# Optimization experiments

Measured on AMD Instinct MI355X. Metric: run time of the kernel, lower is better.

Reference implementation:

```python
import jax, jax.numpy as jnp
import numpy as np

B, S, D, H, NB = 512, 200, 256, 4, 2
DH = D // H
N_ITEMS = 100001  # item_num + 1 (padding idx 0)
EPS = 1e-8


def _ln(x, g, b):
    m = x.mean(-1, keepdims=True)
    v = ((x - m) ** 2).mean(-1, keepdims=True)
    return (x - m) / jnp.sqrt(v + EPS) * g + b


def setup_inputs() -> dict:
    key = jax.random.key(0)
    ks = jax.random.split(key, 20)
    f32 = jnp.float32
    item_emb = jax.random.normal(ks[0], (N_ITEMS, D), f32) * 0.02
    item_emb = item_emb.at[0].set(0.0)  # padding_idx=0
    pos_emb = jax.random.normal(ks[1], (S, D), f32) * 0.02
    inp = {
        'item_emb': item_emb,
        'pos_emb': pos_emb,
        'ln1_g': jnp.ones((NB, D), f32),
        'ln1_b': jnp.zeros((NB, D), f32),
        'in_w': jax.random.normal(ks[2], (NB, 3 * D, D), f32) * 0.02,
        'in_b': jnp.zeros((NB, 3 * D), f32),
        'out_w': jax.random.normal(ks[3], (NB, D, D), f32) * 0.02,
        'out_b': jnp.zeros((NB, D), f32),
        'ln2_g': jnp.ones((NB, D), f32),
        'ln2_b': jnp.zeros((NB, D), f32),
        'c1_w': jax.random.normal(ks[4], (NB, D, D), f32) * 0.02,
        'c1_b': jnp.zeros((NB, D), f32),
        'c2_w': jax.random.normal(ks[5], (NB, D, D), f32) * 0.02,
        'c2_b': jnp.zeros((NB, D), f32),
        'last_g': jnp.ones((D,), f32),
        'last_b': jnp.zeros((D,), f32),
        'user_ids': jax.random.randint(ks[6], (B,), 0, 10000),
        'log_seqs': jax.random.randint(ks[7], (B, S), 0, N_ITEMS),
        'pos_seqs': jax.random.randint(ks[8], (B, S), 0, N_ITEMS),
        'neg_seqs': jax.random.randint(ks[9], (B, S), 0, N_ITEMS),
    }
    return inp


def reference(item_emb, pos_emb, ln1_g, ln1_b, in_w, in_b, out_w, out_b,
              ln2_g, ln2_b, c1_w, c1_b, c2_w, c2_b, last_g, last_b,
              user_ids, log_seqs, pos_seqs, neg_seqs):
    seqs = item_emb[log_seqs] * jnp.asarray(D ** 0.5, item_emb.dtype)
    seqs = seqs + pos_emb[None, :, :]  # positions = arange(S)
    tl_mask = (log_seqs != 0)[..., None].astype(seqs.dtype)  # [B,S,1]
    seqs = seqs * tl_mask
    causal = jnp.tril(jnp.ones((S, S), bool))  # True = attend
    scale = 1.0 / np.sqrt(DH)
    for i in range(NB):
        Q = _ln(seqs, ln1_g[i], ln1_b[i])
        q = (Q @ in_w[i, :D].T + in_b[i, :D]).reshape(B, S, H, DH)
        k = (seqs @ in_w[i, D:2 * D].T + in_b[i, D:2 * D]).reshape(B, S, H, DH)
        v = (seqs @ in_w[i, 2 * D:].T + in_b[i, 2 * D:]).reshape(B, S, H, DH)
        scores = jnp.einsum('bqhd,bkhd->bhqk', q, k) * scale
        scores = jnp.where(causal[None, None], scores, -jnp.inf)
        attn = jax.nn.softmax(scores, axis=-1)
        o = jnp.einsum('bhqk,bkhd->bqhd', attn, v).reshape(B, S, D)
        o = o @ out_w[i].T + out_b[i]
        seqs = Q + o  # residual is on layernormed Q (as in source)
        seqs = _ln(seqs, ln2_g[i], ln2_b[i])
        h1 = jax.nn.relu(seqs @ c1_w[i].T + c1_b[i])
        seqs = (h1 @ c2_w[i].T + c2_b[i] + seqs) * tl_mask
    log_feats = _ln(seqs, last_g, last_b)
    pos_embs = item_emb[pos_seqs]
    neg_embs = item_emb[neg_seqs]
    pos_logits = (log_feats * pos_embs).sum(-1)
    neg_logits = (log_feats * neg_embs).sum(-1)
    return (pos_logits, neg_logits)
```

## Files before the change

kernel.cpp:

```cpp
#include <hip/hip_runtime.h>
#include <math.h>

namespace {

constexpr int kB = 512, kS = 200, kD = 256, kH = 4;
constexpr int kM = kB * kS;
constexpr float kEps = 1e-8f;

typedef short bf16x8 __attribute__((ext_vector_type(8)));
typedef float f32x4 __attribute__((ext_vector_type(4)));

__device__ __forceinline__ float bf2f(unsigned short s) {
  return __uint_as_float(((unsigned)s) << 16);
}
__device__ __forceinline__ unsigned cvtpk(float lo, float hi) {
  unsigned r;
  asm("v_cvt_pk_bf16_f32 %0, %1, %2" : "=v"(r) : "v"(lo), "v"(hi));
  return r;
}
__device__ __forceinline__ void gload16(const void* g, void* l) {
  __builtin_amdgcn_global_load_lds(
      (const __attribute__((address_space(1))) void*)g,
      (__attribute__((address_space(3))) void*)l, 16, 0, 0);
}
__device__ __forceinline__ void vm3() { asm volatile("s_waitcnt vmcnt(3)" ::: "memory"); }
__device__ __forceinline__ void vm2() { asm volatile("s_waitcnt vmcnt(2)" ::: "memory"); }
__device__ __forceinline__ void vm0() { asm volatile("s_waitcnt vmcnt(0)" ::: "memory"); }
__device__ __forceinline__ void lk0() { asm volatile("s_waitcnt lgkmcnt(0)" ::: "memory"); }
__device__ __forceinline__ void bar() { asm volatile("s_barrier" ::: "memory"); }

__global__ __launch_bounds__(256) void cvt4_kernel(
    const float* __restrict__ w0, const float* __restrict__ w1,
    const float* __restrict__ w2, const float* __restrict__ w3,
    const float* __restrict__ ln1g,
    unsigned short* __restrict__ o0, unsigned short* __restrict__ o1,
    unsigned short* __restrict__ o2, unsigned short* __restrict__ o3) {
  int blk = blockIdx.x;
  const float* src;
  unsigned short* dst;
  int base;
  bool isin = false;
  if (blk < 384)      { src = w0; dst = o0; base = blk; isin = true; }
  else if (blk < 512) { src = w1; dst = o1; base = blk - 384; }
  else if (blk < 640) { src = w2; dst = o2; base = blk - 512; }
  else                { src = w3; dst = o3; base = blk - 640; }
  int i4 = (base * 256 + threadIdx.x) * 4;
  float4 v = *reinterpret_cast<const float4*>(src + i4);
  if (isin) {
    int layer = (i4 >= 196608) ? 1 : 0;
    int rem = i4 - layer * 196608;
    int n = rem >> 8;
    int k = rem & 255;
    if (n < 256) {
      float4 g = *reinterpret_cast<const float4*>(ln1g + layer * 256 + k);
      v.x *= g.x; v.y *= g.y; v.z *= g.z; v.w *= g.w;
    }
  }
  uint2 o = {cvtpk(v.x, v.y), cvtpk(v.z, v.w)};
  *reinterpret_cast<uint2*>(dst + i4) = o;
}

__global__ __launch_bounds__(64) void s1s2_kernel(
    const float* __restrict__ in_w, const float* __restrict__ in_b,
    const float* __restrict__ ln1g, const float* __restrict__ ln1b,
    float* __restrict__ s1o, float* __restrict__ s2o) {
  int blk = blockIdx.x;
  int layer = blk >> 8, n = blk & 255;
  int k = threadIdx.x * 4;
  float4 w = *reinterpret_cast<const float4*>(in_w + (size_t)layer * 196608 + n * 256 + k);
  float4 g = *reinterpret_cast<const float4*>(ln1g + layer * 256 + k);
  float4 b = *reinterpret_cast<const float4*>(ln1b + layer * 256 + k);
  float a = w.x * g.x + w.y * g.y + w.z * g.z + w.w * g.w;
  float c = w.x * b.x + w.y * b.y + w.z * b.z + w.w * b.w;
#pragma unroll
  for (int o = 32; o >= 1; o >>= 1) { a += __shfl_xor(a, o); c += __shfl_xor(c, o); }
  if (threadIdx.x == 0) {
    s1o[blk] = a;
    s2o[blk] = c + in_b[layer * 768 + n];
  }
}

__global__ __launch_bounds__(512) void embed_kernel(
    const float* __restrict__ item_emb, const float* __restrict__ pos_emb,
    const int* __restrict__ log_seqs, unsigned short* __restrict__ x,
    float2* __restrict__ stats) {
  int bs = blockIdx.x * 8 + (threadIdx.x >> 6);
  int s = bs % kS;
  int idx = log_seqs[bs];
  float msk = (idx != 0) ? 1.f : 0.f;
  int t = threadIdx.x & 63;
  float4 a = reinterpret_cast<const float4*>(item_emb + (size_t)idx * kD)[t];
  float4 p = reinterpret_cast<const float4*>(pos_emb + (size_t)s * kD)[t];
  float v[4];
  v[0] = (a.x * 16.f + p.x) * msk;
  v[1] = (a.y * 16.f + p.y) * msk;
  v[2] = (a.z * 16.f + p.z) * msk;
  v[3] = (a.w * 16.f + p.w) * msk;
  uint2 r = {cvtpk(v[0], v[1]), cvtpk(v[2], v[3])};
  reinterpret_cast<uint2*>(x + (size_t)bs * kD)[t] = r;
  float sm = v[0] + v[1] + v[2] + v[3];
#pragma unroll
  for (int o = 32; o >= 1; o >>= 1) sm += __shfl_xor(sm, o);
  float mean = sm * (1.f / kD);
  float d0 = v[0] - mean, d1 = v[1] - mean, d2 = v[2] - mean, d3 = v[3] - mean;
  float vs = d0 * d0 + d1 * d1 + d2 * d2 + d3 * d3;
#pragma unroll
  for (int o = 32; o >= 1; o >>= 1) vs += __shfl_xor(vs, o);
  if (t == 0) stats[bs] = {mean, rsqrtf(vs * (1.f / kD) + kEps)};
}

template <int MODE, int LN, int G3>
__global__ __launch_bounds__(512, 4) void gemm2(
    const unsigned short* __restrict__ A, int lda,
    const unsigned short* __restrict__ W,
    const float* __restrict__ bias,
    const unsigned short* __restrict__ R, int ldr,
    const float* __restrict__ lng, const float* __restrict__ lnb,
    const float* __restrict__ qg, const float* __restrict__ qb,
    const float2* __restrict__ statsIn,
    const float* __restrict__ s1v, const float* __restrict__ s2v,
    unsigned short* __restrict__ C, int ldc) {
  __shared__ __attribute__((aligned(16))) unsigned short SMEM[36864];
  __shared__ float red1[128][4];
  __shared__ float red2[128][4];
  const int tid = threadIdx.x, lane = tid & 63, wid = tid >> 6;
  int m0, n0;
  if (G3) {
    int g = blockIdx.x / 24, sub = blockIdx.x % 24;
    m0 = (g * 8 + (sub & 7)) * 128;
    n0 = (sub >> 3) * 256;
  } else {
    m0 = blockIdx.x * 128;
    n0 = 0;
  }
  const int wm = wid >> 2, wn = wid & 3;
  const int lrow = lane & 15, kgrp = lane >> 4;
  const int srow = tid >> 2;
  const int sslot = (tid & 3) ^ (srow & 3);
  const unsigned short* gA  = A + (size_t)(m0 + srow) * lda + sslot * 8;
  const unsigned short* gW0 = W + (size_t)(n0 + srow) * kD + sslot * 8;
  const unsigned short* gW1 = gW0 + (size_t)128 * kD;
  const int sa = (kgrp ^ (lrow & 3)) * 8;

#define STAGE(kk, bb)                                                   \
  do {                                                                  \
    gload16(gA + (kk) * 32, &SMEM[(bb) * 4096 + wid * 512]);            \
    gload16(gW0 + (kk) * 32, &SMEM[12288 + (bb) * 8192 + wid * 512]);   \
    gload16(gW1 + (kk) * 32, &SMEM[16384 + (bb) * 8192 + wid * 512]);   \
  } while (0)

  f32x4 acc[4][4] = {};
  STAGE(0, 0);
  STAGE(1, 1);
#pragma unroll
  for (int k = 0; k < 8; ++k) {
    if (k < 7) vm3(); else vm0();
    bar();
    const int buf = k % 3;
    bf16x8 af[4], bfr[4];
#pragma unroll
    for (int x = 0; x < 4; ++x) {
      af[x]  = *reinterpret_cast<const bf16x8*>(
          &SMEM[12288 + buf * 8192 + (wn * 64 + x * 16 + lrow) * 32 + sa]);
      bfr[x] = *reinterpret_cast<const bf16x8*>(
          &SMEM[buf * 4096 + (wm * 64 + x * 16 + lrow) * 32 + sa]);
    }
    if (k + 2 < 8) STAGE(k + 2, (k + 2) % 3);
    __builtin_amdgcn_s_setprio(1);
#pragma unroll
    for (int na = 0; na < 4; ++na)
#pragma unroll
      for (int mb = 0; mb < 4; ++mb)
        acc[na][mb] = __builtin_amdgcn_mfma_f32_16x16x32_bf16(
            af[na], bfr[mb], acc[na][mb], 0, 0, 0);
    __builtin_amdgcn_s_setprio(0);
  }
#undef STAGE
  __syncthreads();
  const bool qpath = (MODE == 4) && (n0 == 0);
  float2 st[4];
  if (MODE == 5 || (MODE == 4 && n0 == 0)) {
#pragma unroll
    for (int mb = 0; mb < 4; ++mb)
      st[mb] = statsIn[m0 + wm * 64 + mb * 16 + lrow];
  }

  auto computeX = [&](int na, int mb, float x[4]) {
    const int gcol = n0 + wn * 64 + na * 16 + kgrp * 4;
    const f32x4 v = acc[na][mb];
    if (MODE == 4 && qpath) {
      float4 t1 = *reinterpret_cast<const float4*>(s1v + gcol);
      float4 t2 = *reinterpret_cast<const float4*>(s2v + gcol);
      const float s1f[4] = {t1.x, t1.y, t1.z, t1.w};
      const float s2f[4] = {t2.x, t2.y, t2.z, t2.w};
#pragma unroll
      for (int r = 0; r < 4; ++r)
        x[r] = st[mb].y * (v[r] - st[mb].x * s1f[r]) + s2f[r];
      return;
    }
    float4 b4 = *reinterpret_cast<const float4*>(bias + gcol);
    const float bx[4] = {b4.x, b4.y, b4.z, b4.w};
    if (MODE == 4) {
#pragma unroll
      for (int r = 0; r < 4; ++r) x[r] = v[r] + bx[r];
    } else {
      int m = m0 + wm * 64 + mb * 16 + lrow;
      ushort4 rv = *reinterpret_cast<const ushort4*>(R + (size_t)m * ldr + gcol);
      const unsigned short* rs = reinterpret_cast<const unsigned short*>(&rv);
      float4 t1 = *reinterpret_cast<const float4*>(qg + gcol);
      float4 t2 = *reinterpret_cast<const float4*>(qb + gcol);
      const float g4[4] = {t1.x, t1.y, t1.z, t1.w};
      const float qb4[4] = {t2.x, t2.y, t2.z, t2.w};
#pragma unroll
      for (int r = 0; r < 4; ++r) {
        float q = (bf2f(rs[r]) - st[mb].x) * st[mb].y * g4[r] + qb4[r];
        x[r] = v[r] + bx[r] + q;
      }
    }
  };

  float mean[4], inv[4];
  if (LN) {
    float sA[4] = {0.f, 0.f, 0.f, 0.f}, sB[4] = {0.f, 0.f, 0.f, 0.f};
#pragma unroll
    for (int na = 0; na < 4; ++na)
#pragma unroll
      for (int mb = 0; mb < 4; ++mb) {
        float x[4];
        computeX(na, mb, x);
#pragma unroll
        for (int r = 0; r < 4; ++r) { sA[mb] += x[r]; sB[mb] += x[r] * x[r]; }
      }
#pragma unroll
    for (int mb = 0; mb < 4; ++mb) {
      sA[mb] += __shfl_xor(sA[mb], 16); sA[mb] += __shfl_xor(sA[mb], 32);
      sB[mb] += __shfl_xor(sB[mb], 16); sB[mb] += __shfl_xor(sB[mb], 32);
    }
    if (kgrp == 0) {
#pragma unroll
      for (int mb = 0; mb < 4; ++mb) {
        int rl = wm * 64 + mb * 16 + lrow;
        red1[rl][wn] = sA[mb];
        red2[rl][wn] = sB[mb];
      }
    }
    __syncthreads();
#pragma unroll
    for (int mb = 0; mb < 4; ++mb) {
      int rl = wm * 64 + mb * 16 + lrow;
      float4 p1 = *reinterpret_cast<const float4*>(red1[rl]);
      float4 p2 = *reinterpret_cast<const float4*>(red2[rl]);
      float t1 = p1.x + p1.y + p1.z + p1.w;
      float t2 = p2.x + p2.y + p2.z + p2.w;
      float mu = t1 * (1.f / 256.f);
      float var = t2 * (1.f / 256.f) - mu * mu;
      mean[mb] = mu;
      inv[mb] = rsqrtf(fmaxf(var, 0.f) + kEps);
    }
  }

  unsigned short* eb = &SMEM[wid * 3072];
  const int rr = lane >> 2, c8 = (lane & 3) * 8;
#pragma unroll
  for (int hh = 0; hh < 2; ++hh) {
    lk0();
#pragma unroll
    for (int mbl = 0; mbl < 2; ++mbl) {
      int mb = hh * 2 + mbl;
#pragma unroll
      for (int na = 0; na < 4; ++na) {
        float x[4];
        computeX(na, mb, x);
        if (LN == 1) {
          int gcol = n0 + wn * 64 + na * 16 + kgrp * 4;
          float4 g4v = *reinterpret_cast<const float4*>(lng + gcol);
          float4 b4v = *reinterpret_cast<const float4*>(lnb + gcol);
          x[0] = (x[0] - mean[mb]) * inv[mb] * g4v.x + b4v.x;
          x[1] = (x[1] - mean[mb]) * inv[mb] * g4v.y + b4v.y;
          x[2] = (x[2] - mean[mb]) * inv[mb] * g4v.z + b4v.z;
          x[3] = (x[3] - mean[mb]) * inv[mb] * g4v.w + b4v.w;
        }
        uint2 o = {cvtpk(x[0], x[1]), cvtpk(x[2], x[3])};
        *reinterpret_cast<uint2*>(&eb[(mbl * 16 + lrow) * 72 + na * 16 + kgrp * 4]) = o;
      }
    }
    lk0();
#pragma unroll
    for (int rh = 0; rh < 2; ++rh) {
      int row = rh * 16 + rr;
      uint4 d0 = *reinterpret_cast<const uint4*>(&eb[row * 72 + c8]);
      uint4 d1 = *reinterpret_cast<const uint4*>(&eb[row * 72 + 32 + c8]);
      size_t gbase = (size_t)(m0 + wm * 64 + hh * 32 + row) * ldc + (n0 + wn * 64 + c8);
      *reinterpret_cast<uint4*>(C + gbase) = d0;
      *reinterpret_cast<uint4*>(C + gbase + 32) = d1;
    }
  }
}

template <int LAST>
__global__ __launch_bounds__(512, 4) void ffn_fused(
    const unsigned short* __restrict__ A, int lda,
    const unsigned short* __restrict__ W1, const float* __restrict__ b1,
    const unsigned short* __restrict__ W2, const float* __restrict__ b2,
    const int* __restrict__ logseq,
    const float* __restrict__ lng, const float* __restrict__ lnb,
    float2* __restrict__ statsOut,
    const float* __restrict__ iembf, const int* __restrict__ posq,
    const int* __restrict__ negq, float* __restrict__ outlg,
    unsigned short* __restrict__ C, int ldc) {
  __shared__ __attribute__((aligned(16))) unsigned short SMEM[36864];
  __shared__ float red1[64][4];
  __shared__ float red2[64][4];
  const int tid = threadIdx.x, lane = tid & 63, wid = tid >> 6;
  const int m0 = blockIdx.x * 64;
  const int wm = wid >> 2, wn = wid & 3;
  const int lrow = lane & 15, kgrp = lane >> 4;
  unsigned short* As = SMEM;
  unsigned short* Ws = SMEM + 4096;
  unsigned short* H1 = SMEM + 20480;
  const int arow = (wid & 3) * 16 + (lane >> 2);
  const int aslot = (lane & 3) ^ (arow & 3);
  const unsigned short* gA = A + (size_t)(m0 + arow) * lda + aslot * 8;
  const int wrow0 = wid * 32 + (lane >> 2);
  const int wrow1 = wrow0 + 16;
  const int ws0 = (lane & 3) ^ (wrow0 & 3);
  const int ws1 = (lane & 3) ^ (wrow1 & 3);
  const unsigned short* gW10 = W1 + wrow0 * 256 + ws0 * 8;
  const unsigned short* gW11 = W1 + wrow1 * 256 + ws1 * 8;
  const unsigned short* gW20 = W2 + wrow0 * 256 + ws0 * 8;
  const unsigned short* gW21 = W2 + wrow1 * 256 + ws1 * 8;
  const int sa = (kgrp ^ (lrow & 3)) * 8;
  const f32x4 zero = {0.f, 0.f, 0.f, 0.f};

#define STG1(kk, bb)                                               \
  do {                                                             \
    if (wid < 4) gload16(gA + (kk) * 32, &As[(bb) * 2048 + wid * 512]); \
    gload16(gW10 + (kk) * 32, &Ws[(bb) * 8192 + wid * 1024]);      \
    gload16(gW11 + (kk) * 32, &Ws[(bb) * 8192 + wid * 1024 + 512]);\
  } while (0)

  f32x4 acc[4][2] = {};
  STG1(0, 0);
  STG1(1, 1);
#pragma unroll
  for (int k = 0; k < 8; ++k) {
    if (k < 7) { if (wid < 4) vm3(); else vm2(); } else vm0();
    bar();
    const int buf = k & 1;
    bf16x8 af[4], bfr[2];
#pragma unroll
    for (int x = 0; x < 4; ++x)
      af[x] = *reinterpret_cast<const bf16x8*>(
          &Ws[buf * 8192 + (wn * 64 + x * 16 + lrow) * 32 + sa]);
#pragma unroll
    for (int mb = 0; mb < 2; ++mb)
      bfr[mb] = *reinterpret_cast<const bf16x8*>(
          &As[buf * 2048 + (wm * 32 + mb * 16 + lrow) * 32 + sa]);
    __builtin_amdgcn_s_setprio(1);
#pragma unroll
    for (int na = 0; na < 4; ++na)
#pragma unroll
      for (int mb = 0; mb < 2; ++mb)
        acc[na][mb] = __builtin_amdgcn_mfma_f32_16x16x32_bf16(
            af[na], bfr[mb], acc[na][mb], 0, 0, 0);
    __builtin_amdgcn_s_setprio(0);
    bar();
    if (k + 2 < 8) STG1(k + 2, k & 1);
  }
#undef STG1
#pragma unroll
  for (int na = 0; na < 4; ++na) {
    int c0 = wn * 64 + na * 16 + kgrp * 4;
    float4 b4 = *reinterpret_cast<const float4*>(b1 + c0);
#pragma unroll
    for (int mb = 0; mb < 2; ++mb) {
      int row = wm * 32 + mb * 16 + lrow;
      f32x4 v = acc[na][mb];
      float x0 = fmaxf(v[0] + b4.x, 0.f), x1 = fmaxf(v[1] + b4.y, 0.f);
      float x2 = fmaxf(v[2] + b4.z, 0.f), x3 = fmaxf(v[3] + b4.w, 0.f);
      int s = wn * 8 + na * 2 + (kgrp >> 1);
      int addr = row * 256 + ((s ^ (row & 7)) << 3) + (kgrp & 1) * 4;
      uint2 o = {cvtpk(x0, x1), cvtpk(x2, x3)};
      *reinterpret_cast<uint2*>(&H1[addr]) = o;
    }
  }
  __syncthreads();
  ushort4 rres[4][2];
#pragma unroll
  for (int na = 0; na < 4; ++na) {
    int gcol = wn * 64 + na * 16 + kgrp * 4;
#pragma unroll
    for (int mb = 0; mb < 2; ++mb) {
      int m = m0 + wm * 32 + mb * 16 + lrow;
      rres[na][mb] = *reinterpret_cast<const ushort4*>(A + (size_t)m * lda + gcol);
    }
  }
#pragma unroll
  for (int na = 0; na < 4; ++na)
#pragma unroll
    for (int mb = 0; mb < 2; ++mb) acc[na][mb] = zero;

#define STG2(kk, bb)                                               \
  do {                                                             \
    gload16(gW20 + (kk) * 32, &Ws[(bb) * 8192 + wid * 1024]);      \
    gload16(gW21 + (kk) * 32, &Ws[(bb) * 8192 + wid * 1024 + 512]);\
  } while (0)

  STG2(0, 0);
  STG2(1, 1);
#pragma unroll
  for (int k = 0; k < 8; ++k) {
    if (k < 7) vm2(); else vm0();
    bar();
    const int buf = k & 1;
    bf16x8 af[4], bfr[2];
#pragma unroll
    for (int x = 0; x < 4; ++x)
      af[x] = *reinterpret_cast<const bf16x8*>(
          &Ws[buf * 8192 + (wn * 64 + x * 16 + lrow) * 32 + sa]);
#pragma unroll
    for (int mb = 0; mb < 2; ++mb) {
      int row = wm * 32 + mb * 16 + lrow;
      bfr[mb] = *reinterpret_cast<const bf16x8*>(
          &H1[row * 256 + (((k * 4 + kgrp) ^ (row & 7)) << 3)]);
    }
    __builtin_amdgcn_s_setprio(1);
#pragma unroll
    for (int na = 0; na < 4; ++na)
#pragma unroll
      for (int mb = 0; mb < 2; ++mb)
        acc[na][mb] = __builtin_amdgcn_mfma_f32_16x16x32_bf16(
            af[na], bfr[mb], acc[na][mb], 0, 0, 0);
    __builtin_amdgcn_s_setprio(0);
    bar();
    if (k + 2 < 8) STG2(k + 2, k & 1);
  }
#undef STG2
  __syncthreads();

  float msk[2];
#pragma unroll
  for (int mb = 0; mb < 2; ++mb)
    msk[mb] = (logseq[m0 + wm * 32 + mb * 16 + lrow] != 0) ? 1.f : 0.f;

  auto computeY = [&](int na, int mb, float x[4]) {
    int gcol = wn * 64 + na * 16 + kgrp * 4;
    f32x4 v = acc[na][mb];
    float4 b4 = *reinterpret_cast<const float4*>(b2 + gcol);
    const unsigned short* rs = reinterpret_cast<const unsigned short*>(&rres[na][mb]);
    const float bx[4] = {b4.x, b4.y, b4.z, b4.w};
#pragma unroll
    for (int r = 0; r < 4; ++r)
      x[r] = (v[r] + bx[r] + bf2f(rs[r])) * msk[mb];
  };

  if (LAST == 0) {
    f32x4 yv[4][2];
#pragma unroll
    for (int na = 0; na < 4; ++na)
#pragma unroll
      for (int mb = 0; mb < 2; ++mb) {
        float x[4];
        computeY(na, mb, x);
        yv[na][mb][0] = x[0]; yv[na][mb][1] = x[1];
        yv[na][mb][2] = x[2]; yv[na][mb][3] = x[3];
      }
    float sA[2] = {0.f, 0.f}, sB[2] = {0.f, 0.f};
#pragma unroll
    for (int na = 0; na < 4; ++na)
#pragma unroll
      for (int mb = 0; mb < 2; ++mb)
#pragma unroll
        for (int r = 0; r < 4; ++r) {
          float x = yv[na][mb][r];
          sA[mb] += x;
          sB[mb] += x * x;
        }
#pragma unroll
    for (int mb = 0; mb < 2; ++mb) {
      sA[mb] += __shfl_xor(sA[mb], 16); sA[mb] += __shfl_xor(sA[mb], 32);
      sB[mb] += __shfl_xor(sB[mb], 16); sB[mb] += __shfl_xor(sB[mb], 32);
    }
    if (kgrp == 0) {
#pragma unroll
      for (int mb = 0; mb < 2; ++mb) {
        int rl = wm * 32 + mb * 16 + lrow;
        red1[rl][wn] = sA[mb];
        red2[rl][wn] = sB[mb];
      }
    }
    __syncthreads();
    if (wn == 0 && kgrp == 0) {
#pragma unroll
      for (int mb = 0; mb < 2; ++mb) {
        int rl = wm * 32 + mb * 16 + lrow;
        float4 p1 = *reinterpret_cast<const float4*>(red1[rl]);
        float4 p2 = *reinterpret_cast<const float4*>(red2[rl]);
        float t1 = p1.x + p1.y + p1.z + p1.w;
        float t2 = p2.x + p2.y + p2.z + p2.w;
        float mu = t1 * (1.f / 256.f);
        float var = t2 * (1.f / 256.f) - mu * mu;
        statsOut[m0 + rl] = {mu, rsqrtf(fmaxf(var, 0.f) + kEps)};
      }
    }
    unsigned short* eb = &SMEM[wid * 2560];
#pragma unroll
    for (int mb = 0; mb < 2; ++mb)
#pragma unroll
      for (int na = 0; na < 4; ++na) {
        uint2 o = {cvtpk(yv[na][mb][0], yv[na][mb][1]),
                   cvtpk(yv[na][mb][2], yv[na][mb][3])};
        *reinterpret_cast<uint2*>(&eb[(mb * 16 + lrow) * 72 + na * 16 + kgrp * 4]) = o;
      }
    lk0();
#pragma unroll
    for (int rh = 0; rh < 4; ++rh) {
      int row = rh * 8 + (lane >> 3);
      uint4 d = *reinterpret_cast<const uint4*>(&eb[row * 72 + (lane & 7) * 8]);
      *reinterpret_cast<uint4*>(
          C + (size_t)(m0 + wm * 32 + row) * ldc + wn * 64 + (lane & 7) * 8) = d;
    }
    return;
  }

  float* SL = reinterpret_cast<float*>(SMEM);
  int pi[2], ni[2];
#pragma unroll
  for (int mb = 0; mb < 2; ++mb) {
    int m = m0 + wm * 32 + mb * 16 + lrow;
    pi[mb] = posq[m];
    ni[mb] = negq[m];
  }
#pragma unroll
  for (int mb = 0; mb < 2; ++mb) {
    float4 peL[4], neL[4];
#pragma unroll
    for (int na = 0; na < 4; ++na) {
      int gcol = wn * 64 + na * 16 + kgrp * 4;
      peL[na] = *reinterpret_cast<const float4*>(iembf + (size_t)pi[mb] * 256 + gcol);
      neL[na] = *reinterpret_cast<const float4*>(iembf + (size_t)ni[mb] * 256 + gcol);
    }
    float sa_ = 0.f, sb_ = 0.f;
    float s1p = 0.f, s2p = 0.f, s3p = 0.f;
    float s1n = 0.f, s2n = 0.f, s3n = 0.f;
#pragma unroll
    for (int na = 0; na < 4; ++na) {
      float x[4];
      computeY(na, mb, x);
      int gcol = wn * 64 + na * 16 + kgrp * 4;
      float4 g4v = *reinterpret_cast<const float4*>(lng + gcol);
      float4 b4v = *reinterpret_cast<const float4*>(lnb + gcol);
      const float gg[4] = {g4v.x, g4v.y, g4v.z, g4v.w};
      const float lb[4] = {b4v.x, b4v.y, b4v.z, b4v.w};
      const float pef[4] = {peL[na].x, peL[na].y, peL[na].z, peL[na].w};
      const float nef[4] = {neL[na].x, neL[na].y, neL[na].z, neL[na].w};
#pragma unroll
      for (int r = 0; r < 4; ++r) {
        sa_ += x[r];
        sb_ += x[r] * x[r];
        float gp = gg[r] * pef[r], gn = gg[r] * nef[r];
        s1p += x[r] * gp; s2p += gp; s3p += lb[r] * pef[r];
        s1n += x[r] * gn; s2n += gn; s3n += lb[r] * nef[r];
      }
    }
    float vals[8] = {sa_, sb_, s1p, s2p, s3p, s1n, s2n, s3n};
#pragma unroll
    for (int j = 0; j < 8; ++j) {
      vals[j] += __shfl_xor(vals[j], 16);
      vals[j] += __shfl_xor(vals[j], 32);
    }
    if (kgrp == 0) {
      int rl = wm * 32 + mb * 16 + lrow;
      float* dst = &SL[rl * 33 + wn * 8];
#pragma unroll
      for (int j = 0; j < 8; ++j) dst[j] = vals[j];
    }
  }
  __syncthreads();
  if (tid < 64) {
    float t[8] = {0.f, 0.f, 0.f, 0.f, 0.f, 0.f, 0.f, 0.f};
#pragma unroll
    for (int w = 0; w < 4; ++w) {
      const float* src = &SL[tid * 33 + w * 8];
#pragma unroll
      for (int j = 0; j < 8; ++j) t[j] += src[j];
    }
    float mean = t[0] * (1.f / 256.f);
    float var = t[1] * (1.f / 256.f) - mean * mean;
    float inv = rsqrtf(fmaxf(var, 0.f) + kEps);
    int m = m0 + tid;
    outlg[m] = inv * (t[2] - mean * t[3]) + t[4];
    outlg[(size_t)kM + m] = inv * (t[5] - mean * t[6]) + t[7];
  }
}

__global__ __launch_bounds__(512) void attn_mfma(unsigned short* __restrict__ qkv) {
  constexpr int kVS = 232, kQS = 768;
  __shared__ __attribute__((aligned(16))) unsigned short Kl[200 * 64];
  __shared__ __attribute__((aligned(16))) unsigned short Vt[64 * kVS];
  __shared__ __attribute__((aligned(16))) unsigned short Pt[8 * 636];
  int bid = blockIdx.x;
  int h = (bid >> 3) & 3;
  int b = (bid & 7) | ((bid >> 5) << 3);
  int tid = threadIdx.x, lane = tid & 63, wid = tid >> 6;
  const unsigned short* kvb = qkv + (size_t)b * kS * kQS + 256 + h * 64;
  for (int i = tid; i < 1600; i += 512) {
    int row = i >> 3, slot = i & 7;
    *reinterpret_cast<uint4*>(&Kl[row * 64 + ((slot ^ (row & 7)) << 3)]) =
        *reinterpret_cast<const uint4*>(kvb + (size_t)row * kQS + slot * 8);
  }
  for (int i = tid; i < 3200; i += 512) {
    int row = i >> 4, d0 = (i & 15) * 4;
    ushort4 v = *reinterpret_cast<const ushort4*>(kvb + 256 + (size_t)row * kQS + d0);
    Vt[(d0 + 0) * kVS + row] = v.x;
    Vt[(d0 + 1) * kVS + row] = v.y;
    Vt[(d0 + 2) * kVS + row] = v.z;
    Vt[(d0 + 3) * kVS + row] = v.w;
  }
  for (int i = tid; i < 2048; i += 512) {
    int d = i >> 5, c = i & 31;
    Vt[d * kVS + 200 + c] = 0;
  }
  __syncthreads();

  int qcol = lane & 15, kgrp = lane >> 4;
  const float scale2 = 0.18033688f;
  int packed = (wid < 3) ? (0xFFFC - wid) : (0xFF09 + (wid - 3) * 15);
  unsigned short* ptw = &Pt[wid * 636];
#pragma unroll
  for (int ti = 0; ti < 2; ++ti) {
    int t = (packed >> (ti * 4)) & 15;
    if (t == 15) break;
    int qb = t * 16;
    int qrow = qb + qcol;
    int qm = min(qrow, kS - 1);
    const unsigned short* qrp = qkv + (size_t)(b * kS + qm) * kQS + h * 64;
    bf16x8 qf0 = *reinterpret_cast<const bf16x8*>(qrp + kgrp * 8);
    bf16x8 qf1 = *reinterpret_cast<const bf16x8*>(qrp + 32 + kgrp * 8);
    f32x4 accO[4] = {};
    float l_run = 0.f;
    int nc = (qb + 47) >> 5;
    for (int c = 0; c < nc; ++c) {
      int kbase = c * 32;
      f32x4 s0 = {}, s1 = {};
      int kr0 = min(kbase + qcol, kS - 1);
      int kr1 = min(kbase + 16 + qcol, kS - 1);
      const unsigned short* K0a = &Kl[kr0 * 64 + ((kgrp ^ (kr0 & 7)) << 3)];
      const unsigned short* K0b = &Kl[kr0 * 64 + (((kgrp + 4) ^ (kr0 & 7)) << 3)];
      const unsigned short* K1a = &Kl[kr1 * 64 + ((kgrp ^ (kr1 & 7)) << 3)];
      const unsigned short* K1b = &Kl[kr1 * 64 + (((kgrp + 4) ^ (kr1 & 7)) << 3)];
      s0 = __builtin_amdgcn_mfma_f32_16x16x32_bf16(*reinterpret_cast<const bf16x8*>(K0a), qf0, s0, 0, 0, 0);
      s0 = __builtin_amdgcn_mfma_f32_16x16x32_bf16(*reinterpret_cast<const bf16x8*>(K0b), qf1, s0, 0, 0, 0);
      s1 = __builtin_amdgcn_mfma_f32_16x16x32_bf16(*reinterpret_cast<const bf16x8*>(K1a), qf0, s1, 0, 0, 0);
      s1 = __builtin_amdgcn_mfma_f32_16x16x32_bf16(*reinterpret_cast<const bf16x8*>(K1b), qf1, s1, 0, 0, 0);
      float p[8];
      float psum = 0.f;
#pragma unroll
      for (int r = 0; r < 4; ++r) {
        int key0 = kbase + kgrp * 4 + r;
        int key1 = key0 + 16;
        float x0 = (key0 <= qm) ? fmaf(s0[r], scale2, -8.f) : -3.0e38f;
        float x1 = (key1 <= qm) ? fmaf(s1[r], scale2, -8.f) : -3.0e38f;
        p[r] = exp2f(x0);
        p[r + 4] = exp2f(x1);
        psum += p[r] + p[r + 4];
      }
      l_run += psum;
      uint2 w0 = {cvtpk(p[0], p[1]), cvtpk(p[2], p[3])};
      uint2 w1 = {cvtpk(p[4], p[5]), cvtpk(p[6], p[7])};
      *reinterpret_cast<uint2*>(&ptw[qcol * 40 + kgrp * 4]) = w0;
      *reinterpret_cast<uint2*>(&ptw[qcol * 40 + 16 + kgrp * 4]) = w1;
      bf16x8 pf = *reinterpret_cast<const bf16x8*>(&ptw[qcol * 40 + kgrp * 8]);
#pragma unroll
      for (int nf = 0; nf < 4; ++nf) {
        bf16x8 vf = *reinterpret_cast<const bf16x8*>(
            &Vt[(nf * 16 + qcol) * kVS + kbase + kgrp * 8]);
        accO[nf] = __builtin_amdgcn_mfma_f32_16x16x32_bf16(vf, pf, accO[nf], 0, 0, 0);
      }
    }
    float l_tot = l_run;
    l_tot += __shfl_xor(l_tot, 16);
    l_tot += __shfl_xor(l_tot, 32);
    float inv = 1.f / l_tot;
    if (qrow < kS) {
      unsigned short* op = qkv + (size_t)(b * kS + qrow) * kQS + h * 64;
#pragma unroll
      for (int nf = 0; nf < 4; ++nf) {
        uint2 o4 = {cvtpk(accO[nf][0] * inv, accO[nf][1] * inv),
                    cvtpk(accO[nf][2] * inv, accO[nf][3] * inv)};
        *reinterpret_cast<uint2*>(op + nf * 16 + kgrp * 4) = o4;
      }
    }
  }
}

}

extern "C" void kernel_launch(void* const* d_in, const int* in_sizes, int n_in,
                              void* d_out, int out_size, void* d_ws,
                              size_t ws_size, hipStream_t stream) {
  const float* item_emb = (const float*)d_in[0];
  const float* pos_emb  = (const float*)d_in[1];
  const float* ln1_g = (const float*)d_in[2];
  const float* ln1_b = (const float*)d_in[3];
  const float* in_w  = (const float*)d_in[4];
  const float* in_b  = (const float*)d_in[5];
  const float* out_w = (const float*)d_in[6];
  const float* out_b = (const float*)d_in[7];
  const float* ln2_g = (const float*)d_in[8];
  const float* ln2_b = (const float*)d_in[9];
  const float* c1_w  = (const float*)d_in[10];
  const float* c1_b  = (const float*)d_in[11];
  const float* c2_w  = (const float*)d_in[12];
  const float* c2_b  = (const float*)d_in[13];
  const float* last_g = (const float*)d_in[14];
  const float* last_b = (const float*)d_in[15];
  const int* log_seqs = (const int*)d_in[17];
  const int* pos_seqs = (const int*)d_in[18];
  const int* neg_seqs = (const int*)d_in[19];
  float* out = (float*)d_out;

  size_t unit = (size_t)kM * kD;
  unsigned short* X   = (unsigned short*)d_ws;
  unsigned short* QKV = X + unit;
  unsigned short* inw_bf  = X + 4 * unit;
  unsigned short* outw_bf = inw_bf + 2 * 768 * 256;
  unsigned short* c1w_bf  = outw_bf + 2 * 256 * 256;
  unsigned short* c2w_bf  = c1w_bf + 2 * 256 * 256;
  float2* stats = (float2*)(c2w_bf + 2 * 256 * 256);
  float* s1buf = (float*)(stats + 2 * kM);
  float* s2buf = s1buf + 512;

  cvt4_kernel<<<768, 256, 0, stream>>>(in_w, out_w, c1_w, c2_w, ln1_g,
                                       inw_bf, outw_bf, c1w_bf, c2w_bf);
  s1s2_kernel<<<512, 64, 0, stream>>>(in_w, in_b, ln1_g, ln1_b, s1buf, s2buf);
  embed_kernel<<<kM / 8, 512, 0, stream>>>(item_emb, pos_emb, log_seqs, X, stats);

  dim3 g1(kM / 128, 1);
  for (int l = 0; l < 2; ++l) {
    const unsigned short* iw = inw_bf + (size_t)l * 768 * 256;
    float2* stl = stats + (size_t)l * kM;
    gemm2<4, 0, 1><<<kM / 128 * 3, 512, 0, stream>>>(
        X, 256, iw, in_b + l * 768, nullptr, 0,
        nullptr, nullptr, nullptr, nullptr, stl,
        s1buf + l * 256, s2buf + l * 256, QKV, 768);
    attn_mfma<<<kB * kH, 512, 0, stream>>>(QKV);
    gemm2<5, 1, 0><<<g1, 512, 0, stream>>>(
        QKV, 768, outw_bf + (size_t)l * kD * kD, out_b + l * kD, X, 256,
        ln2_g + l * kD, ln2_b + l * kD, ln1_g + l * kD, ln1_b + l * kD,
        stl, nullptr, nullptr, QKV + 256, 768);
    if (l == 0) {
      ffn_fused<0><<<kM / 64, 512, 0, stream>>>(
          QKV + 256, 768, c1w_bf, c1_b, c2w_bf, c2_b, log_seqs,
          nullptr, nullptr, stats + kM, nullptr, nullptr, nullptr, nullptr,
          X, 256);
    } else {
      ffn_fused<1><<<kM / 64, 512, 0, stream>>>(
          QKV + 256, 768, c1w_bf + 65536, c1_b + 256, c2w_bf + 65536, c2_b + 256,
          log_seqs, last_g, last_b, nullptr, item_emb, pos_seqs, neg_seqs, out,
          nullptr, 0);
    }
  }
}
```

Measured before the change: 617.3 us.

## Shrink FFN shared memory: preload full A tile, single-buffer weights, reuse for H1

The fused FFN kernel now loads the whole 64x256 activation tile into shared memory once, reuses that same region for the H1 intermediate, and reads the residual from LDS instead of global memory. Weight tiles become single-buffered with a full vmcnt(0) wait each k-step, and launch bounds are raised to 6 blocks per CU. The aim is lower LDS use (48KB vs 72KB) and higher occupancy, at the cost of the previous double-buffered prefetch overlap, so every iteration now waits on its weight load.

New measurement: 656.8 us. 6.4% more time.

```diff
diff --git a/kernel.cpp b/kernel.cpp
--- a/kernel.cpp
+++ b/kernel.cpp
@@ -24,7 +24,6 @@
       (__attribute__((address_space(3))) void*)l, 16, 0, 0);
 }
 __device__ __forceinline__ void vm3() { asm volatile("s_waitcnt vmcnt(3)" ::: "memory"); }
-__device__ __forceinline__ void vm2() { asm volatile("s_waitcnt vmcnt(2)" ::: "memory"); }
 __device__ __forceinline__ void vm0() { asm volatile("s_waitcnt vmcnt(0)" ::: "memory"); }
 __device__ __forceinline__ void lk0() { asm volatile("s_waitcnt lgkmcnt(0)" ::: "memory"); }
 __device__ __forceinline__ void bar() { asm volatile("s_barrier" ::: "memory"); }
@@ -298,7 +297,7 @@
 }
 
 template <int LAST>
-__global__ __launch_bounds__(512, 4) void ffn_fused(
+__global__ __launch_bounds__(512, 6) void ffn_fused(
     const unsigned short* __restrict__ A, int lda,
     const unsigned short* __restrict__ W1, const float* __restrict__ b1,
     const unsigned short* __restrict__ W2, const float* __restrict__ b2,
@@ -308,19 +307,22 @@
     const float* __restrict__ iembf, const int* __restrict__ posq,
     const int* __restrict__ negq, float* __restrict__ outlg,
     unsigned short* __restrict__ C, int ldc) {
-  __shared__ __attribute__((aligned(16))) unsigned short SMEM[36864];
+  __shared__ __attribute__((aligned(16))) unsigned short SMEM[24576];
   __shared__ float red1[64][4];
   __shared__ float red2[64][4];
   const int tid = threadIdx.x, lane = tid & 63, wid = tid >> 6;
   const int m0 = blockIdx.x * 64;
   const int wm = wid >> 2, wn = wid & 3;
   const int lrow = lane & 15, kgrp = lane >> 4;
-  unsigned short* As = SMEM;
-  unsigned short* Ws = SMEM + 4096;
-  unsigned short* H1 = SMEM + 20480;
-  const int arow = (wid & 3) * 16 + (lane >> 2);
-  const int aslot = (lane & 3) ^ (arow & 3);
-  const unsigned short* gA = A + (size_t)(m0 + arow) * lda + aslot * 8;
+  unsigned short* Wb = SMEM + 16384;
+  {
+    const int arw = tid >> 5;
+    const int asl = (tid & 31) ^ (arw & 7);
+    const unsigned short* gAr = A + (size_t)(m0 + arw) * lda + asl * 8;
+#pragma unroll
+    for (int p = 0; p < 4; ++p)
+      gload16(gAr + (size_t)(p * 16) * lda, &SMEM[p * 4096 + wid * 512]);
+  }
   const int wrow0 = wid * 32 + (lane >> 2);
   const int wrow1 = wrow0 + 16;
   const int ws0 = (lane & 3) ^ (wrow0 & 3);
@@ -332,30 +334,24 @@
   const int sa = (kgrp ^ (lrow & 3)) * 8;
   const f32x4 zero = {0.f, 0.f, 0.f, 0.f};
 
-#define STG1(kk, bb)                                               \
-  do {                                                             \
-    if (wid < 4) gload16(gA + (kk) * 32, &As[(bb) * 2048 + wid * 512]); \
-    gload16(gW10 + (kk) * 32, &Ws[(bb) * 8192 + wid * 1024]);      \
-    gload16(gW11 + (kk) * 32, &Ws[(bb) * 8192 + wid * 1024 + 512]);\
-  } while (0)
-
   f32x4 acc[4][2] = {};
-  STG1(0, 0);
-  STG1(1, 1);
 #pragma unroll
   for (int k = 0; k < 8; ++k) {
-    if (k < 7) { if (wid < 4) vm3(); else vm2(); } else vm0();
+    gload16(gW10 + k * 32, &Wb[wid * 1024]);
+    gload16(gW11 + k * 32, &Wb[wid * 1024 + 512]);
+    vm0();
     bar();
-    const int buf = k & 1;
     bf16x8 af[4], bfr[2];
 #pragma unroll
     for (int x = 0; x < 4; ++x)
       af[x] = *reinterpret_cast<const bf16x8*>(
-          &Ws[buf * 8192 + (wn * 64 + x * 16 + lrow) * 32 + sa]);
-#pragma unroll
-    for (int mb = 0; mb < 2; ++mb)
+          &Wb[(wn * 64 + x * 16 + lrow) * 32 + sa]);
+#pragma unroll
+    for (int mb = 0; mb < 2; ++mb) {
+      int row = wm * 32 + mb * 16 + lrow;
       bfr[mb] = *reinterpret_cast<const bf16x8*>(
-          &As[buf * 2048 + (wm * 32 + mb * 16 + lrow) * 32 + sa]);
+          &SMEM[row * 256 + (((k * 4 + kgrp) ^ (row & 7)) << 3)]);
+    }
     __builtin_amdgcn_s_setprio(1);
 #pragma unroll
     for (int na = 0; na < 4; ++na)
@@ -365,64 +361,56 @@
             af[na], bfr[mb], acc[na][mb], 0, 0, 0);
     __builtin_amdgcn_s_setprio(0);
     bar();
-    if (k + 2 < 8) STG1(k + 2, k & 1);
-  }
-#undef STG1
+  }
+  uint2 rres[4][2];
+#pragma unroll
+  for (int na = 0; na < 4; ++na) {
+    int s = wn * 8 + na * 2 + (kgrp >> 1);
+#pragma unroll
+    for (int mb = 0; mb < 2; ++mb) {
+      int row = wm * 32 + mb * 16 + lrow;
+      rres[na][mb] = *reinterpret_cast<const uint2*>(
+          &SMEM[row * 256 + ((s ^ (row & 7)) << 3) + (kgrp & 1) * 4]);
+    }
+  }
+  lk0();
 #pragma unroll
   for (int na = 0; na < 4; ++na) {
     int c0 = wn * 64 + na * 16 + kgrp * 4;
     float4 b4 = *reinterpret_cast<const float4*>(b1 + c0);
+    int s = wn * 8 + na * 2 + (kgrp >> 1);
 #pragma unroll
     for (int mb = 0; mb < 2; ++mb) {
       int row = wm * 32 + mb * 16 + lrow;
       f32x4 v = acc[na][mb];
       float x0 = fmaxf(v[0] + b4.x, 0.f), x1 = fmaxf(v[1] + b4.y, 0.f);
       float x2 = fmaxf(v[2] + b4.z, 0.f), x3 = fmaxf(v[3] + b4.w, 0.f);
-      int s = wn * 8 + na * 2 + (kgrp >> 1);
-      int addr = row * 256 + ((s ^ (row & 7)) << 3) + (kgrp & 1) * 4;
       uint2 o = {cvtpk(x0, x1), cvtpk(x2, x3)};
-      *reinterpret_cast<uint2*>(&H1[addr]) = o;
+      *reinterpret_cast<uint2*>(
+          &SMEM[row * 256 + ((s ^ (row & 7)) << 3) + (kgrp & 1) * 4]) = o;
     }
   }
   __syncthreads();
-  ushort4 rres[4][2];
-#pragma unroll
-  for (int na = 0; na < 4; ++na) {
-    int gcol = wn * 64 + na * 16 + kgrp * 4;
-#pragma unroll
-    for (int mb = 0; mb < 2; ++mb) {
-      int m = m0 + wm * 32 + mb * 16 + lrow;
-      rres[na][mb] = *reinterpret_cast<const ushort4*>(A + (size_t)m * lda + gcol);
-    }
-  }
 #pragma unroll
   for (int na = 0; na < 4; ++na)
 #pragma unroll
     for (int mb = 0; mb < 2; ++mb) acc[na][mb] = zero;
-
-#define STG2(kk, bb)                                               \
-  do {                                                             \
-    gload16(gW20 + (kk) * 32, &Ws[(bb) * 8192 + wid * 1024]);      \
-    gload16(gW21 + (kk) * 32, &Ws[(bb) * 8192 + wid * 1024 + 512]);\
-  } while (0)
-
-  STG2(0, 0);
-  STG2(1, 1);
 #pragma unroll
   for (int k = 0; k < 8; ++k) {
-    if (k < 7) vm2(); else vm0();
+    gload16(gW20 + k * 32, &Wb[wid * 1024]);
+    gload16(gW21 + k * 32, &Wb[wid * 1024 + 512]);
+    vm0();
     bar();
-    const int buf = k & 1;
     bf16x8 af[4], bfr[2];
 #pragma unroll
     for (int x = 0; x < 4; ++x)
       af[x] = *reinterpret_cast<const bf16x8*>(
-          &Ws[buf * 8192 + (wn * 64 + x * 16 + lrow) * 32 + sa]);
+          &Wb[(wn * 64 + x * 16 + lrow) * 32 + sa]);
 #pragma unroll
     for (int mb = 0; mb < 2; ++mb) {
       int row = wm * 32 + mb * 16 + lrow;
       bfr[mb] = *reinterpret_cast<const bf16x8*>(
-          &H1[row * 256 + (((k * 4 + kgrp) ^ (row & 7)) << 3)]);
+          &SMEM[row * 256 + (((k * 4 + kgrp) ^ (row & 7)) << 3)]);
     }
     __builtin_amdgcn_s_setprio(1);
 #pragma unroll
@@ -433,9 +421,7 @@
             af[na], bfr[mb], acc[na][mb], 0, 0, 0);
     __builtin_amdgcn_s_setprio(0);
     bar();
-    if (k + 2 < 8) STG2(k + 2, k & 1);
-  }
-#undef STG2
+  }
   __syncthreads();
 
   float msk[2];
```
